# Kernel tuning notes

Measured on AMD Instinct MI355X. Metric: run time of the kernel, lower is better.

## Reference

```python
import jax, jax.numpy as jnp
import numpy as np

HID = 128
MAX_NODES = 100000
MAX_EDGES = 300000
EVT_LEN = 4096
NUM_NODE = 20000
NUM_EDGE = 320000
# EVENT_TYPE_ID_MAP: pad=0 start=1 end=2 node-add=3 node-delete=4 edge-add=5 edge-delete=6
NODE_ADD, NODE_DEL = 3, 4


def time_encode(t, time_w, time_b):
    # TimeEncoder: cos(Linear(1 -> hidden)(t))
    return jnp.cos(t[..., None] * time_w + time_b)


def gru_cell(x, h, w_ih, w_hh, b_ih, b_hh):
    gi = x @ w_ih.T + b_ih
    gh = h @ w_hh.T + b_hh
    i_r, i_z, i_n = jnp.split(gi, 3, axis=-1)
    h_r, h_z, h_n = jnp.split(gh, 3, axis=-1)
    r = jax.nn.sigmoid(i_r + h_r)
    z = jax.nn.sigmoid(i_z + h_z)
    n = jnp.tanh(i_n + r * h_n)
    return (1.0 - z) * n + z * h


def setup_inputs() -> dict:
    key = jax.random.key(0)
    ks = jax.random.split(key, 32)
    H = HID
    s = 0.05
    inp = {}
    inp["event_type_ids"] = jax.random.randint(ks[0], (EVT_LEN,), 0, 7)
    inp["src_ids"] = jax.random.randint(ks[1], (EVT_LEN,), 0, MAX_NODES)
    inp["src_mask"] = (jax.random.uniform(ks[2], (EVT_LEN,)) > 0.3).astype(jnp.float32)
    inp["dst_ids"] = jax.random.randint(ks[3], (EVT_LEN,), 0, MAX_NODES)
    inp["dst_mask"] = (jax.random.uniform(ks[4], (EVT_LEN,)) > 0.3).astype(jnp.float32)
    inp["event_edge_ids"] = jax.random.randint(ks[5], (EVT_LEN,), 0, MAX_EDGES)
    inp["event_embeddings"] = jax.random.normal(ks[6], (EVT_LEN, H), dtype=jnp.float32)
    inp["event_mask"] = (jax.random.uniform(ks[7], (EVT_LEN,)) > 0.2).astype(jnp.float32)
    inp["event_timestamps"] = jax.random.uniform(ks[8], (EVT_LEN,)) * 100.0
    inp["node_ids"] = jax.random.randint(ks[9], (NUM_NODE,), 0, MAX_NODES)
    inp["edge_ids"] = jax.random.randint(ks[10], (NUM_EDGE,), 0, MAX_EDGES)
    inp["edge_index"] = jax.random.randint(ks[11], (2, NUM_EDGE), 0, NUM_NODE)
    inp["time"] = 100
    # persistent-buffer state
    inp["memory"] = jax.random.normal(ks[12], (MAX_NODES, H), dtype=jnp.float32) * s
    inp["last_update"] = jax.random.uniform(ks[13], (MAX_EDGES,)) * 50.0
    inp["node_features"] = jax.random.normal(ks[14], (MAX_NODES, H), dtype=jnp.float32) * s
    inp["edge_features"] = jax.random.normal(ks[15], (MAX_EDGES, H), dtype=jnp.float32) * s
    # TimeEncoder params (Linear(1, H))
    inp["time_w"] = jax.random.normal(ks[16], (H,), dtype=jnp.float32) * s
    inp["time_b"] = jax.random.normal(ks[17], (H,), dtype=jnp.float32) * s
    # GRUCell(5H -> H)
    inp["gru_w_ih"] = jax.random.normal(ks[18], (3 * H, 5 * H), dtype=jnp.float32) * s
    inp["gru_w_hh"] = jax.random.normal(ks[19], (3 * H, H), dtype=jnp.float32) * s
    inp["gru_b_ih"] = jax.random.normal(ks[20], (3 * H,), dtype=jnp.float32) * s
    inp["gru_b_hh"] = jax.random.normal(ks[21], (3 * H,), dtype=jnp.float32) * s
    # TransformerConv(H, H, heads=1, edge_dim=2H)
    inp["wq"] = jax.random.normal(ks[22], (H, H), dtype=jnp.float32) * s
    inp["bq"] = jax.random.normal(ks[23], (H,), dtype=jnp.float32) * s
    inp["wk"] = jax.random.normal(ks[24], (H, H), dtype=jnp.float32) * s
    inp["bk"] = jax.random.normal(ks[25], (H,), dtype=jnp.float32) * s
    inp["wv"] = jax.random.normal(ks[26], (H, H), dtype=jnp.float32) * s
    inp["bv"] = jax.random.normal(ks[27], (H,), dtype=jnp.float32) * s
    inp["we"] = jax.random.normal(ks[28], (H, 2 * H), dtype=jnp.float32) * s  # lin_edge, no bias
    inp["wskip"] = jax.random.normal(ks[29], (H, H), dtype=jnp.float32) * s
    inp["bskip"] = jax.random.normal(ks[30], (H,), dtype=jnp.float32) * s
    return inp


def reference(event_type_ids, src_ids, src_mask, dst_ids, dst_mask, event_edge_ids,
              event_embeddings, event_mask, event_timestamps, node_ids, edge_ids,
              edge_index, time, memory, last_update, node_features, edge_features,
              time_w, time_b, gru_w_ih, gru_w_hh, gru_b_ih, gru_b_hh,
              wq, bq, wk, bk, wv, bv, we, wskip, bskip):
    H = HID
    # ---- message() ----
    L = event_type_ids.shape[0]
    type_embs = jnp.broadcast_to(event_type_ids[:, None].astype(memory.dtype), (L, H))
    src_embs = memory[src_ids] * src_mask[:, None]
    dst_embs = memory[dst_ids] * dst_mask[:, None]
    edge_last = last_update[event_edge_ids]
    rel_ts = event_timestamps - edge_last * dst_mask
    is_node_ev = ((event_type_ids == NODE_ADD) | (event_type_ids == NODE_DEL)).astype(event_timestamps.dtype)
    ts_emb = time_encode(event_timestamps * is_node_ev + rel_ts * dst_mask, time_w, time_b) * event_mask[:, None]
    src_msgs = jnp.concatenate([type_embs, src_embs, dst_embs, ts_emb, event_embeddings], axis=1) * event_mask[:, None]
    dst_msgs = jnp.concatenate([type_embs, dst_embs, src_embs, ts_emb, event_embeddings], axis=1) * dst_mask[:, None]
    # ---- agg_message(): scatter-mean over node ids ----
    def agg(msgs, ids):
        s = jax.ops.segment_sum(msgs, ids, num_segments=MAX_NODES)
        c = jax.ops.segment_sum(jnp.ones((msgs.shape[0],), msgs.dtype), ids, num_segments=MAX_NODES)
        return s / jnp.maximum(c, 1.0)[:, None]
    agg_src = agg(src_msgs, src_ids)
    agg_dst = agg(dst_msgs, dst_ids)
    # ---- GRU memory update on unique ids ----
    # torch: memory[cat(uniq_src, uniq_dst)] = rnn(...); reads use pre-update memory,
    # dst writes come after src writes so they override on overlap. Duplicate ids in
    # src_ids carry identical per-id values, so scatter-set is equivalent to unique().
    new_src = gru_cell(agg_src[src_ids], memory[src_ids], gru_w_ih, gru_w_hh, gru_b_ih, gru_b_hh)
    new_dst = gru_cell(agg_dst[dst_ids], memory[dst_ids], gru_w_ih, gru_w_hh, gru_b_ih, gru_b_hh)
    memory = memory.at[src_ids].set(new_src)
    memory = memory.at[dst_ids].set(new_dst)
    # ---- edge attributes ----
    rel_t = time - last_update[edge_ids]
    rel_t_embs = time_encode(rel_t, time_w, time_b)
    edge_attr = jnp.concatenate([rel_t_embs, edge_features[edge_ids]], axis=-1)  # (E, 2H)
    # ---- TransformerConv (heads=1, concat, root_weight) ----
    x = node_features[node_ids] + memory[node_ids]  # (N, H)
    src, dst = edge_index[0], edge_index[1]
    q = x @ wq.T + bq
    k = x @ wk.T + bk
    v = x @ wv.T + bv
    e = edge_attr @ we.T  # lin_edge (no bias)
    alpha = jnp.sum(q[dst] * (k[src] + e), axis=-1) / jnp.sqrt(jnp.asarray(H, x.dtype))
    amax = jax.ops.segment_max(alpha, dst, num_segments=x.shape[0])
    ex = jnp.exp(alpha - amax[dst])
    denom = jax.ops.segment_sum(ex, dst, num_segments=x.shape[0])
    p = ex / jnp.maximum(denom[dst], 1e-16)
    out = jax.ops.segment_sum(p[:, None] * (v[src] + e), dst, num_segments=x.shape[0])
    return out + x @ wskip.T + bskip
```

## Files before the change

### kernel.cpp

```cpp
#include <hip/hip_runtime.h>
#include <math.h>

#define HID   128
#define MAXN  100000
#define MAXE  300000
#define EVT   4096
#define NNODE 20000
#define NEDGE 320000

typedef unsigned short u16;
typedef __attribute__((ext_vector_type(8))) short bf16x8;
typedef __attribute__((ext_vector_type(4))) float f32x4;

#define OFF_WCATB     0u
#define OFF_WEB       589824u
#define OFF_WALLB     655360u
#define OFF_BALL      851968u
#define BASE2         855040u
#define OFF_HEAD_SRC  (BASE2 + 0u)
#define OFF_HEAD_DST  (BASE2 + 400128u)
#define OFF_CNT_SRC   (BASE2 + 800256u)
#define OFF_CNT_DST   (BASE2 + 1200384u)
#define OFF_CHAIN_SRC (BASE2 + 1600512u)
#define OFF_CHAIN_DST (BASE2 + 1616896u)
#define OFF_XHB       (BASE2 + 1703936u)
#define OFF_HG        (BASE2 + 14286848u)
#define OFF_GRZ       (BASE2 + 20000000u)
#define OFF_GIN       (BASE2 + 28388608u)
#define OFF_GHN       (BASE2 + 32582912u)
#define OFF_XB        (BASE2 + 20000000u)
#define OFF_QB        (BASE2 + 25120000u)
#define OFF_SKIPF     (BASE2 + 55840000u)
#define OFF_DEG       (BASE2 + 66080000u)
#define OFF_OFFS      (BASE2 + 66160128u)
#define OFF_CURSOR    (BASE2 + 66240256u)
#define OFF_SORTED    (BASE2 + 66320384u)
#define OFF_SACCB     (BASE2 + 67600384u)

__device__ __forceinline__ float sigmoidf_(float x) { return 1.f / (1.f + __expf(-x)); }
__device__ __forceinline__ u16 f2b(float f) {
    unsigned u = __float_as_uint(f);
    unsigned r = (u + 0x7fffu + ((u >> 16) & 1u)) >> 16;
    return (u16)r;
}
__device__ __forceinline__ float b2f(unsigned h) { return __uint_as_float(h << 16); }

__global__ void k_prep(const float* __restrict__ w_ih, const float* __restrict__ w_hh,
                       const float* __restrict__ we,
                       const float* __restrict__ wq, const float* __restrict__ wk_,
                       const float* __restrict__ wv, const float* __restrict__ wskip,
                       const float* __restrict__ bq, const float* __restrict__ bk,
                       const float* __restrict__ bv, const float* __restrict__ bskip,
                       u16* __restrict__ Wcatb, u16* __restrict__ we_b,
                       u16* __restrict__ Wallb, float* __restrict__ ball,
                       int* __restrict__ deg, char* __restrict__ zbase) {
    int b = blockIdx.x, t = threadIdx.x;
    if (b < 1152) {
        int idx = b * 256 + t;
        int row = idx / 768, col = idx % 768;
        float v = (col < 640) ? w_ih[row * 640 + col] : w_hh[row * 128 + (col - 640)];
        Wcatb[idx] = f2b(v);
        return;
    }
    b -= 1152;
    if (b < 128) {
        int i = b * 256 + t;
        we_b[i] = f2b(we[i]);
        return;
    }
    b -= 128;
    if (b < 79) {
        int i = b * 256 + t;
        if (i < NNODE) deg[i] = 0;
        return;
    }
    b -= 79;
    if (b < 384) {
        int idx = b * 256 + t;
        int row = idx >> 7;
        int k = idx & 127;
        float v;
        if (row < 128)      v = wq[row * 128 + k];
        else if (row < 256) v = wk_[(row - 128) * 128 + k];
        else if (row < 384) v = wv[(row - 256) * 128 + k];
        else if (row < 512) v = wskip[(row - 384) * 128 + k];
        else {
            int j = row - 512;
            float a = 0.f;
            for (int t2 = 0; t2 < 128; t2++) a += wq[t2 * 128 + k] * we[t2 * 256 + j];
            v = a;
        }
        Wallb[row * 128 + k] = f2b(v);
        if (k == 0) {
            float bb;
            if (row < 128)      bb = bq[row];
            else if (row < 256) bb = bk[row - 128];
            else if (row < 384) bb = bv[row - 256];
            else if (row < 512) bb = bskip[row - 384];
            else { int j = row - 512; float a = 0.f; for (int t2 = 0; t2 < 128; t2++) a += bq[t2] * we[t2 * 256 + j]; bb = a; }
            ball[row] = bb;
        }
        return;
    }
    b -= 384;
    const int NFF = 50016;
    uint4 ff = make_uint4(0xFFFFFFFFu, 0xFFFFFFFFu, 0xFFFFFFFFu, 0xFFFFFFFFu);
    uint4 zz = make_uint4(0u, 0u, 0u, 0u);
    int idx = b * 256 + t;
    int stride = 257 * 256;
    uint4* pff = (uint4*)zbase;
    uint4* pzz = (uint4*)(zbase + 800256);
    for (int i = idx; i < NFF; i += stride) pff[i] = ff;
    for (int i = idx; i < NFF; i += stride) pzz[i] = zz;
}

__global__ void k_msg_tables(const int* __restrict__ et_ids, const int* __restrict__ src_ids,
                          const float* __restrict__ src_mask, const int* __restrict__ dst_ids,
                          const float* __restrict__ dst_mask, const int* __restrict__ ev_eids,
                          const float* __restrict__ ev_emb, const float* __restrict__ ev_mask,
                          const float* __restrict__ ev_ts, const float* __restrict__ memory,
                          const float* __restrict__ last_update, const float* __restrict__ time_w,
                          const float* __restrict__ time_b,
                          int* __restrict__ head_src, int* __restrict__ head_dst,
                          int* __restrict__ cnt_src, int* __restrict__ cnt_dst,
                          int* __restrict__ chain_src, int* __restrict__ chain_dst,
                          const int* __restrict__ eidx, int* __restrict__ deg,
                          u16* __restrict__ XHb, float* __restrict__ Hg) {
    int b = blockIdx.x, t = threadIdx.x;
    if (b >= EVT) {
        int bb = b - EVT;
        if (bb < 32) {
            int i = bb * 128 + t;
            int s = src_ids[i], d = dst_ids[i];
            chain_src[i] = atomicExch(&head_src[s], i);
            atomicAdd(&cnt_src[s], 1);
            chain_dst[i] = atomicExch(&head_dst[d], i);
            atomicAdd(&cnt_dst[d], 1);
        } else {
            int j = (bb - 32) * 128 + t;
            atomicAdd(&deg[eidx[NEDGE + j]], 1);
        }
        return;
    }
    int i = b;
    int c = t;
    int et = et_ids[i];
    float sm = src_mask[i], dm = dst_mask[i], em = ev_mask[i], ts = ev_ts[i];
    int sid = src_ids[i], did = dst_ids[i], eid = ev_eids[i];
    float isnode = (et == 3 || et == 4) ? 1.f : 0.f;
    float rel = ts - last_update[eid] * dm;
    float tval = ts * isnode + rel * dm;
    float tse = __cosf(tval * time_w[c] + time_b[c]) * em;
    float typ = (float)et;
    float sv_raw = memory[(size_t)sid * HID + c];
    float dv_raw = memory[(size_t)did * HID + c];
    float sv = sv_raw * sm;
    float dv = dv_raw * dm;
    float ev = ev_emb[(size_t)i * HID + c];
    Hg[(size_t)i * HID + c] = sv_raw;
    Hg[(size_t)(EVT + i) * HID + c] = dv_raw;
    u16* xs = XHb + (size_t)i * 768;
    xs[c] = f2b(typ * em); xs[128 + c] = f2b(sv * em); xs[256 + c] = f2b(dv * em);
    xs[384 + c] = f2b(tse * em); xs[512 + c] = f2b(ev * em);
    xs[640 + c] = f2b(sv_raw);
    u16* xd = XHb + (size_t)(EVT + i) * 768;
    xd[c] = f2b(typ * dm); xd[128 + c] = f2b(dv * dm); xd[256 + c] = f2b(sv * dm);
    xd[384 + c] = f2b(tse * dm); xd[512 + c] = f2b(ev * dm);
    xd[640 + c] = f2b(dv_raw);
}

__global__ void k_fix(const int* __restrict__ src_ids, const int* __restrict__ dst_ids,
                      const int* __restrict__ head_src, const int* __restrict__ head_dst,
                      const int* __restrict__ chain_src, const int* __restrict__ chain_dst,
                      const int* __restrict__ cnt_src, const int* __restrict__ cnt_dst,
                      const int* __restrict__ et_ids, const float* __restrict__ src_mask,
                      const float* __restrict__ dst_mask, const int* __restrict__ ev_eids,
                      const float* __restrict__ ev_emb, const float* __restrict__ ev_mask,
                      const float* __restrict__ ev_ts, const float* __restrict__ memory,
                      const float* __restrict__ last_update, const float* __restrict__ time_w,
                      const float* __restrict__ time_b, u16* __restrict__ XHb) {
    int r = blockIdx.x, c = threadIdx.x;
    bool is_src = (r < EVT);
    int id = is_src ? src_ids[r] : dst_ids[r - EVT];
    int cnt = is_src ? cnt_src[id] : cnt_dst[id];
    if (cnt < 2) return;
    float own = memory[(size_t)id * HID + c];
    float tw = time_w[c], tb = time_b[c];
    float a0 = 0.f, a1 = 0.f, a2 = 0.f, a3 = 0.f, a4 = 0.f;
    int j = is_src ? head_src[id] : head_dst[id];
    for (int k = 0; k < cnt; ++k) {
        int et = et_ids[j];
        float sm = src_mask[j], dm = dst_mask[j], em = ev_mask[j], ts = ev_ts[j];
        int eid = ev_eids[j];
        float isnode = (et == 3 || et == 4) ? 1.f : 0.f;
        float rel = ts - last_update[eid] * dm;
        float tval = ts * isnode + rel * dm;
        float tse = __cosf(tval * tw + tb);
        float ev = ev_emb[(size_t)j * HID + c];
        float typ = (float)et;
        if (is_src) {
            float sv = own * sm;
            float dv = memory[(size_t)dst_ids[j] * HID + c] * dm;
            float tsm = tse * em;
            a0 += typ * em; a1 += sv * em; a2 += dv * em;
            a3 += tsm * em; a4 += ev * em;
            j = chain_src[j];
        } else {
            float dv = own * dm;
            float sv = memory[(size_t)src_ids[j] * HID + c] * sm;
            float tsm = tse * em;
            a0 += typ * dm; a1 += dv * dm; a2 += sv * dm;
            a3 += tsm * dm; a4 += ev * dm;
            j = chain_dst[j];
        }
    }
    float inv = 1.f / (float)cnt;
    u16* x = XHb + (size_t)r * 768;
    x[c] = f2b(a0 * inv); x[128 + c] = f2b(a1 * inv); x[256 + c] = f2b(a2 * inv);
    x[384 + c] = f2b(a3 * inv); x[512 + c] = f2b(a4 * inv);
}

__device__ __forceinline__ void gate_pass(const u16* __restrict__ A, int lda,
                                          const u16* __restrict__ W, int ldw, int K,
                                          f32x4 acc[4][4], u16* Als, u16* Wls,
                                          int bm, int wm, int wn, int l15, int quad, int tid) {
    for (int k0 = 0; k0 < K; k0 += 32) {
#pragma unroll
        for (int h = 0; h < 2; ++h) {
            int ch = tid + h * 256;
            int row = ch >> 2, kc = (ch & 3) * 8;
            *(float4*)&Als[row * 40 + kc] = *(const float4*)(A + (size_t)(bm + row) * lda + k0 + kc);
            *(float4*)&Wls[row * 40 + kc] = *(const float4*)(W + (size_t)row * ldw + k0 + kc);
        }
        __syncthreads();
        bf16x8 af[4], bfr[4];
#pragma unroll
        for (int r = 0; r < 4; ++r)
            af[r] = *(const bf16x8*)&Als[(wm + r * 16 + l15) * 40 + quad * 8];
#pragma unroll
        for (int c2 = 0; c2 < 4; ++c2)
            bfr[c2] = *(const bf16x8*)&Wls[(wn + c2 * 16 + l15) * 40 + quad * 8];
#pragma unroll
        for (int r = 0; r < 4; ++r)
#pragma unroll
            for (int c2 = 0; c2 < 4; ++c2)
                acc[r][c2] = __builtin_amdgcn_mfma_f32_16x16x32_bf16(af[r], bfr[c2], acc[r][c2], 0, 0, 0);
        __syncthreads();
    }
}

__global__ __launch_bounds__(256) void k_gemm_gates(const u16* __restrict__ XHb,
        const u16* __restrict__ Wcat, const float* __restrict__ b_ih,
        const float* __restrict__ b_hh, float* __restrict__ Grz,
        float* __restrict__ Gin, float* __restrict__ Ghn) {
    __shared__ u16 Als[128 * 40];
    __shared__ u16 Wls[128 * 40];
    int tid = threadIdx.x;
    int bm = blockIdx.x * 128;
    int g = blockIdx.y;
    int wave = tid >> 6, lane = tid & 63;
    int wm = (wave & 1) * 64, wn = (wave >> 1) * 64;
    int l15 = lane & 15, quad = lane >> 4;
    f32x4 acc_i[4][4] = {};
    f32x4 acc_h[4][4] = {};
    const u16* Wg = Wcat + (size_t)(g * 128) * 768;
    gate_pass(XHb, 768, Wg, 768, 640, acc_i, Als, Wls, bm, wm, wn, l15, quad, tid);
    gate_pass(XHb + 640, 768, Wg + 640, 768, 128, acc_h, Als, Wls, bm, wm, wn, l15, quad, tid);
#pragma unroll
    for (int r = 0; r < 4; ++r) {
#pragma unroll
        for (int c2 = 0; c2 < 4; ++c2) {
            int ncol = wn + c2 * 16 + l15;
            float bi = b_ih[g * 128 + ncol];
            float bh = b_hh[g * 128 + ncol];
#pragma unroll
            for (int reg = 0; reg < 4; ++reg) {
                int mrow = bm + wm + r * 16 + quad * 4 + reg;
                if (g < 2) {
                    Grz[(size_t)mrow * 256 + g * 128 + ncol] =
                        acc_i[r][c2][reg] + acc_h[r][c2][reg] + bi + bh;
                } else {
                    Gin[(size_t)mrow * 128 + ncol] = acc_i[r][c2][reg] + bi;
                    Ghn[(size_t)mrow * 128 + ncol] = acc_h[r][c2][reg] + bh;
                }
            }
        }
    }
}

__global__ void k_gru_scatter(const float* __restrict__ Grz, const float* __restrict__ Gin,
                              const float* __restrict__ Ghn, const float* __restrict__ Hg,
                              const int* __restrict__ src_ids, const int* __restrict__ dst_ids,
                              const int* __restrict__ cnt_dst, float* __restrict__ memory) {
    int r = blockIdx.x, c = threadIdx.x;
    float rg = sigmoidf_(Grz[(size_t)r * 256 + c]);
    float z  = sigmoidf_(Grz[(size_t)r * 256 + 128 + c]);
    float n  = tanhf(Gin[(size_t)r * 128 + c] + rg * Ghn[(size_t)r * 128 + c]);
    float h0 = Hg[(size_t)r * HID + c];
    float h  = (1.f - z) * n + z * h0;
    if (r < EVT) {
        int sid = src_ids[r];
        if (cnt_dst[sid] == 0) memory[(size_t)sid * HID + c] = h;
    } else {
        int did = dst_ids[r - EVT];
        memory[(size_t)did * HID + c] = h;
    }
}

__device__ __forceinline__ void gemm_tile(const u16* __restrict__ A, const u16* __restrict__ W,
                                          const float* __restrict__ bias, float* __restrict__ C,
                                          int M, int N, int K, int acc,
                                          u16* Als, u16* Wls) {
    int tid = threadIdx.x;
    int bm = blockIdx.x * 128, bn = blockIdx.y * 128;
    int wave = tid >> 6, lane = tid & 63;
    int wm = (wave & 1) * 64, wn = (wave >> 1) * 64;
    int l15 = lane & 15, quad = lane >> 4;
    f32x4 accf[4][4] = {};
    for (int k0 = 0; k0 < K; k0 += 32) {
#pragma unroll
        for (int h = 0; h < 2; ++h) {
            int ch = tid + h * 256;
            int row = ch >> 2, kc = (ch & 3) * 8;
            int gr = bm + row;
            float4 av = make_float4(0.f, 0.f, 0.f, 0.f);
            if (gr < M) av = *(const float4*)(A + (size_t)gr * K + k0 + kc);
            *(float4*)&Als[row * 40 + kc] = av;
            int wr = bn + row;
            float4 wv_ = *(const float4*)(W + (size_t)wr * K + k0 + kc);
            *(float4*)&Wls[row * 40 + kc] = wv_;
        }
        __syncthreads();
        bf16x8 af[4], bfr[4];
#pragma unroll
        for (int r = 0; r < 4; ++r)
            af[r] = *(const bf16x8*)&Als[(wm + r * 16 + l15) * 40 + quad * 8];
#pragma unroll
        for (int c2 = 0; c2 < 4; ++c2)
            bfr[c2] = *(const bf16x8*)&Wls[(wn + c2 * 16 + l15) * 40 + quad * 8];
#pragma unroll
        for (int r = 0; r < 4; ++r)
#pragma unroll
            for (int c2 = 0; c2 < 4; ++c2)
                accf[r][c2] = __builtin_amdgcn_mfma_f32_16x16x32_bf16(af[r], bfr[c2], accf[r][c2], 0, 0, 0);
        __syncthreads();
    }
#pragma unroll
    for (int r = 0; r < 4; ++r) {
#pragma unroll
        for (int c2 = 0; c2 < 4; ++c2) {
            int ncol = bn + wn + c2 * 16 + l15;
            float bv = bias ? bias[ncol] : 0.f;
#pragma unroll
            for (int reg = 0; reg < 4; ++reg) {
                int mrow = bm + wm + r * 16 + quad * 4 + reg;
                if (mrow >= M) continue;
                float v = accf[r][c2][reg] + bv;
                if (acc) v += C[(size_t)mrow * N + ncol];
                C[(size_t)mrow * N + ncol] = v;
            }
        }
    }
}

__global__ __launch_bounds__(256) void k_gemm_mfma(const u16* __restrict__ A,
                                                   const u16* __restrict__ W,
                                                   const float* __restrict__ bias,
                                                   float* __restrict__ C,
                                                   int M, int N, int K, int acc) {
    __shared__ u16 Als[128 * 40];
    __shared__ u16 Wls[128 * 40];
    gemm_tile(A, W, bias, C, M, N, K, acc, Als, Wls);
}

__global__ __launch_bounds__(256) void k_gemm_qkvse(const u16* __restrict__ A,
                                                    const u16* __restrict__ W,
                                                    const float* __restrict__ bias,
                                                    u16* __restrict__ QB,
                                                    float* __restrict__ SkipF,
                                                    const int* __restrict__ eidx,
                                                    int* __restrict__ cursor,
                                                    int* __restrict__ sorted) {
    __shared__ u16 Als[128 * 40];
    __shared__ u16 Wls[128 * 40];
    if (blockIdx.y == 6) {
        int j = blockIdx.x * 256 + threadIdx.x;
        for (; j < NEDGE; j += 157 * 256) {
            int d = eidx[NEDGE + j];
            int pos = atomicAdd(&cursor[d], 1);
            sorted[pos] = j;
        }
        return;
    }
    int tid = threadIdx.x;
    int bm = blockIdx.x * 128, bn = blockIdx.y * 128;
    int wave = tid >> 6, lane = tid & 63;
    int wm = (wave & 1) * 64, wn = (wave >> 1) * 64;
    int l15 = lane & 15, quad = lane >> 4;
    f32x4 accf[4][4] = {};
    for (int k0 = 0; k0 < 128; k0 += 32) {
#pragma unroll
        for (int h = 0; h < 2; ++h) {
            int ch = tid + h * 256;
            int row = ch >> 2, kc = (ch & 3) * 8;
            int gr = bm + row;
            float4 av = make_float4(0.f, 0.f, 0.f, 0.f);
            if (gr < NNODE) av = *(const float4*)(A + (size_t)gr * 128 + k0 + kc);
            *(float4*)&Als[row * 40 + kc] = av;
            int wr = bn + row;
            float4 wv_ = *(const float4*)(W + (size_t)wr * 128 + k0 + kc);
            *(float4*)&Wls[row * 40 + kc] = wv_;
        }
        __syncthreads();
        bf16x8 af[4], bfr[4];
#pragma unroll
        for (int r = 0; r < 4; ++r)
            af[r] = *(const bf16x8*)&Als[(wm + r * 16 + l15) * 40 + quad * 8];
#pragma unroll
        for (int c2 = 0; c2 < 4; ++c2)
            bfr[c2] = *(const bf16x8*)&Wls[(wn + c2 * 16 + l15) * 40 + quad * 8];
#pragma unroll
        for (int r = 0; r < 4; ++r)
#pragma unroll
            for (int c2 = 0; c2 < 4; ++c2)
                accf[r][c2] = __builtin_amdgcn_mfma_f32_16x16x32_bf16(af[r], bfr[c2], accf[r][c2], 0, 0, 0);
        __syncthreads();
    }
#pragma unroll
    for (int r = 0; r < 4; ++r) {
#pragma unroll
        for (int c2 = 0; c2 < 4; ++c2) {
            int ncol = bn + wn + c2 * 16 + l15;
            float bv = bias[ncol];
#pragma unroll
            for (int reg = 0; reg < 4; ++reg) {
                int mrow = bm + wm + r * 16 + quad * 4 + reg;
                if (mrow >= NNODE) continue;
                float v = accf[r][c2][reg] + bv;
                QB[(size_t)mrow * 768 + ncol] = f2b(v);
                if (ncol >= 384 && ncol < 512)
                    SkipF[(size_t)mrow * 128 + (ncol - 384)] = v;
            }
        }
    }
}

__global__ __launch_bounds__(1024) void k_x_scan(const int* __restrict__ node_ids,
                                                 const float* __restrict__ nf,
                                                 const float* __restrict__ memory,
                                                 u16* __restrict__ Xb,
                                                 const int* __restrict__ deg,
                                                 int* __restrict__ offs,
                                                 int* __restrict__ cursor) {
    __shared__ int wsum[16];
    int p = blockIdx.x, t = threadIdx.x;
    if (p < 2500) {
        int row = p * 8 + (t >> 7), c = t & 127;
        int nid = node_ids[row];
        Xb[(size_t)row * HID + c] = f2b(nf[(size_t)nid * HID + c] + memory[(size_t)nid * HID + c]);
        return;
    }
    int lane = t & 63, w = t >> 6;
    int carry = 0;
    const int N4 = NNODE / 4;
    for (int base = 0; base < N4; base += 1024) {
        int i4 = base + t;
        int4 v = make_int4(0, 0, 0, 0);
        if (i4 < N4) v = ((const int4*)deg)[i4];
        int s = v.x + v.y + v.z + v.w;
        int x = s;
#pragma unroll
        for (int d = 1; d < 64; d <<= 1) { int y = __shfl_up(x, d, 64); if (lane >= d) x += y; }
        if (lane == 63) wsum[w] = x;
        __syncthreads();
        int add = 0, tot = 0;
        for (int k2 = 0; k2 < 16; ++k2) { int ss = wsum[k2]; if (k2 < w) add += ss; tot += ss; }
        if (i4 < N4) {
            int e = carry + add + x - s;
            int4 o;
            o.x = e;
            o.y = e + v.x;
            o.z = o.y + v.y;
            o.w = o.z + v.z;
            ((int4*)offs)[i4] = o;
            ((int4*)cursor)[i4] = o;
        }
        carry += tot;
        __syncthreads();
    }
    if (t == 0) offs[NNODE] = NEDGE;
}

__global__ __launch_bounds__(256) void k_node(const u16* __restrict__ QB,
        const float* __restrict__ SkipF, const int* __restrict__ offs,
        const int* __restrict__ sorted, const int* __restrict__ eidx,
        const int* __restrict__ edge_ids, const float* __restrict__ last_update,
        const float* __restrict__ time_w, const float* __restrict__ time_b,
        const float* __restrict__ ef, const int* __restrict__ tptr,
        float* __restrict__ out, u16* __restrict__ saccb) {
    int wave = threadIdx.x >> 6, lane = threadIdx.x & 63;
    int n = blockIdx.x * 4 + wave;
    int c = 2 * lane;
    const u16* rowq = QB + (size_t)n * 768;
    unsigned qw  = *(const unsigned*)(rowq + c);
    unsigned qtw = *(const unsigned*)(rowq + 512 + c);
    unsigned qfw = *(const unsigned*)(rowq + 640 + c);
    float2 qd, qet, qef;
    qd.x  = b2f(qw & 0xffffu);  qd.y  = b2f(qw >> 16);
    qet.x = b2f(qtw & 0xffffu); qet.y = b2f(qtw >> 16);
    qef.x = b2f(qfw & 0xffffu); qef.y = b2f(qfw >> 16);
    float2 skip = *(const float2*)(SkipF + (size_t)n * HID + c);
    float2 tw   = *(const float2*)(time_w + c);
    float2 tb   = *(const float2*)(time_b + c);
    float tf = (float)(*tptr);
    int start = offs[n], end = offs[n + 1];
    int deg = end - start;
    if (deg == 0) {
        *(float2*)(out + (size_t)n * HID + c) = skip;
        *(unsigned*)(saccb + (size_t)n * 256 + c) = 0u;
        *(unsigned*)(saccb + (size_t)n * 256 + 128 + c) = 0u;
        return;
    }
    float m = -1e30f, l_ = 0.f;
    float va0 = 0.f, va1 = 0.f, s00 = 0.f, s01 = 0.f, s10 = 0.f, s11 = 0.f;
    for (int cb = start; cb < end; cb += 64) {
        int cnt = end - cb; if (cnt > 64) cnt = 64;
        int s_l = 0, eid_l = 0; float rt_l = 0.f;
        if (lane < cnt) {
            int j = sorted[cb + lane];
            s_l = eidx[j];
            eid_l = edge_ids[j];
            rt_l = tf - last_update[eid_l];
        }
        for (int e0 = 0; e0 < cnt; e0 += 4) {
            float pv[4], cv0[4], cv1[4], vx[4], vy[4], ex[4], ey[4];
#pragma unroll
            for (int i = 0; i < 4; ++i) {
                int idx = e0 + i;
                int sel = (idx < cnt) ? idx : e0;
                int s   = __shfl(s_l, sel, 64);
                int eid = __shfl(eid_l, sel, 64);
                float rt = __shfl(rt_l, sel, 64);
                unsigned kvp = *(const unsigned*)(QB + (size_t)s * 768 + 128 + c);
                unsigned vvp = *(const unsigned*)(QB + (size_t)s * 768 + 256 + c);
                float2 ev = *(const float2*)(ef + (size_t)eid * HID + c);
                float k0f = b2f(kvp & 0xffffu), k1f = b2f(kvp >> 16);
                vx[i] = b2f(vvp & 0xffffu); vy[i] = b2f(vvp >> 16);
                cv0[i] = __cosf(rt * tw.x + tb.x);
                cv1[i] = __cosf(rt * tw.y + tb.y);
                ex[i] = ev.x; ey[i] = ev.y;
                pv[i] = qd.x * k0f + qd.y * k1f + qet.x * cv0[i] + qet.y * cv1[i]
                      + qef.x * ev.x + qef.y * ev.y;
            }
#pragma unroll
            for (int msk = 32; msk > 0; msk >>= 1) {
#pragma unroll
                for (int i = 0; i < 4; ++i) pv[i] += __shfl_xor(pv[i], msk, 64);
            }
            float al[4];
#pragma unroll
            for (int i = 0; i < 4; ++i)
                al[i] = (e0 + i < cnt) ? pv[i] * 0.08838834764831845f : -1e30f;
            float gm = fmaxf(fmaxf(al[0], al[1]), fmaxf(al[2], al[3]));
            if (gm > m) {
                float fac = __expf(m - gm);
                l_ *= fac; va0 *= fac; va1 *= fac;
                s00 *= fac; s01 *= fac; s10 *= fac; s11 *= fac;
                m = gm;
            }
#pragma unroll
            for (int i = 0; i < 4; ++i) {
                float w = __expf(al[i] - m);
                l_ += w;
                va0 += w * vx[i]; va1 += w * vy[i];
                s00 += w * cv0[i]; s01 += w * cv1[i];
                s10 += w * ex[i]; s11 += w * ey[i];
            }
        }
    }
    float inv = 1.f / fmaxf(l_, 1e-16f);
    float2 o; o.x = va0 * inv + skip.x; o.y = va1 * inv + skip.y;
    *(float2*)(out + (size_t)n * HID + c) = o;
    unsigned p0 = (unsigned)f2b(s00 * inv) | ((unsigned)f2b(s01 * inv) << 16);
    unsigned p1 = (unsigned)f2b(s10 * inv) | ((unsigned)f2b(s11 * inv) << 16);
    *(unsigned*)(saccb + (size_t)n * 256 + c) = p0;
    *(unsigned*)(saccb + (size_t)n * 256 + 128 + c) = p1;
}

extern "C" void kernel_launch(void* const* d_in, const int* in_sizes, int n_in,
                              void* d_out, int out_size, void* d_ws, size_t ws_size,
                              hipStream_t stream) {
    const int*   et_ids        = (const int*)d_in[0];
    const int*   src_ids       = (const int*)d_in[1];
    const float* src_mask      = (const float*)d_in[2];
    const int*   dst_ids       = (const int*)d_in[3];
    const float* dst_mask      = (const float*)d_in[4];
    const int*   ev_eids       = (const int*)d_in[5];
    const float* ev_emb        = (const float*)d_in[6];
    const float* ev_mask       = (const float*)d_in[7];
    const float* ev_ts         = (const float*)d_in[8];
    const int*   node_ids      = (const int*)d_in[9];
    const int*   edge_ids      = (const int*)d_in[10];
    const int*   edge_index    = (const int*)d_in[11];
    const int*   tptr          = (const int*)d_in[12];
    float*       memory        = (float*)d_in[13];
    const float* last_update   = (const float*)d_in[14];
    const float* node_features = (const float*)d_in[15];
    const float* edge_features = (const float*)d_in[16];
    const float* time_w        = (const float*)d_in[17];
    const float* time_b        = (const float*)d_in[18];
    const float* w_ih          = (const float*)d_in[19];
    const float* w_hh          = (const float*)d_in[20];
    const float* b_ih          = (const float*)d_in[21];
    const float* b_hh          = (const float*)d_in[22];
    const float* wq            = (const float*)d_in[23];
    const float* bq            = (const float*)d_in[24];
    const float* wk            = (const float*)d_in[25];
    const float* bk            = (const float*)d_in[26];
    const float* wv            = (const float*)d_in[27];
    const float* bv            = (const float*)d_in[28];
    const float* we            = (const float*)d_in[29];
    const float* wskip         = (const float*)d_in[30];
    const float* bskip         = (const float*)d_in[31];
    float* out = (float*)d_out;
    char*  wsb = (char*)d_ws;

    u16*   Wcatb    = (u16*)(wsb + OFF_WCATB);
    u16*   we_b     = (u16*)(wsb + OFF_WEB);
    u16*   Wallb    = (u16*)(wsb + OFF_WALLB);
    float* ball     = (float*)(wsb + OFF_BALL);
    int*   head_src = (int*)(wsb + OFF_HEAD_SRC);
    int*   head_dst = (int*)(wsb + OFF_HEAD_DST);
    int*   cnt_src  = (int*)(wsb + OFF_CNT_SRC);
    int*   cnt_dst  = (int*)(wsb + OFF_CNT_DST);
    int*   chain_src= (int*)(wsb + OFF_CHAIN_SRC);
    int*   chain_dst= (int*)(wsb + OFF_CHAIN_DST);
    u16*   XHb      = (u16*)(wsb + OFF_XHB);
    float* Hg       = (float*)(wsb + OFF_HG);
    float* Grz      = (float*)(wsb + OFF_GRZ);
    float* Gin      = (float*)(wsb + OFF_GIN);
    float* Ghn      = (float*)(wsb + OFF_GHN);
    u16*   Xb       = (u16*)(wsb + OFF_XB);
    u16*   QB       = (u16*)(wsb + OFF_QB);
    float* SkipF    = (float*)(wsb + OFF_SKIPF);
    int*   deg      = (int*)(wsb + OFF_DEG);
    int*   offs     = (int*)(wsb + OFF_OFFS);
    int*   cursor   = (int*)(wsb + OFF_CURSOR);
    int*   sorted   = (int*)(wsb + OFF_SORTED);
    u16*   saccb    = (u16*)(wsb + OFF_SACCB);

    k_prep<<<2000, 256, 0, stream>>>(w_ih, w_hh, we, wq, wk, wv, wskip, bq, bk, bv, bskip,
                                     Wcatb, we_b, Wallb, ball, deg, wsb + OFF_HEAD_SRC);
    k_msg_tables<<<6628, 128, 0, stream>>>(et_ids, src_ids, src_mask, dst_ids, dst_mask, ev_eids,
                                           ev_emb, ev_mask, ev_ts, memory, last_update, time_w, time_b,
                                           head_src, head_dst, cnt_src, cnt_dst, chain_src, chain_dst,
                                           edge_index, deg, XHb, Hg);
    k_fix<<<2 * EVT, 128, 0, stream>>>(src_ids, dst_ids, head_src, head_dst, chain_src, chain_dst,
                                       cnt_src, cnt_dst, et_ids, src_mask, dst_mask, ev_eids,
                                       ev_emb, ev_mask, ev_ts, memory, last_update, time_w, time_b,
                                       XHb);
    k_gemm_gates<<<dim3(64, 3), 256, 0, stream>>>(XHb, Wcatb, b_ih, b_hh, Grz, Gin, Ghn);
    k_gru_scatter<<<2 * EVT, 128, 0, stream>>>(Grz, Gin, Ghn, Hg, src_ids, dst_ids, cnt_dst, memory);
    k_x_scan<<<2501, 1024, 0, stream>>>(node_ids, node_features, memory, Xb, deg, offs, cursor);
    k_gemm_qkvse<<<dim3(157, 7), 256, 0, stream>>>(Xb, Wallb, ball, QB, SkipF,
                                                   edge_index, cursor, sorted);
    k_node<<<NNODE / 4, 256, 0, stream>>>(QB, SkipF, offs, sorted, edge_index, edge_ids,
                                          last_update, time_w, time_b, edge_features, tptr,
                                          out, saccb);
    k_gemm_mfma<<<dim3(157, 1), 256, 0, stream>>>(saccb, we_b, nullptr, out, NNODE, 128, 256, 1);
}
```

Before: 480.8 us.

## Move skip projection from QKV GEMM into final edge-projection GEMM

```diff
diff --git a/kernel.cpp b/kernel.cpp
--- a/kernel.cpp
+++ b/kernel.cpp
@@ -15,7 +15,8 @@
 #define OFF_WCATB     0u
 #define OFF_WEB       589824u
 #define OFF_WALLB     655360u
-#define OFF_BALL      851968u
+#define OFF_BALL      819200u
+#define OFF_WSKIPB    821760u
 #define BASE2         855040u
 #define OFF_HEAD_SRC  (BASE2 + 0u)
 #define OFF_HEAD_DST  (BASE2 + 400128u)
@@ -30,7 +31,6 @@
 #define OFF_GHN       (BASE2 + 32582912u)
 #define OFF_XB        (BASE2 + 20000000u)
 #define OFF_QB        (BASE2 + 25120000u)
-#define OFF_SKIPF     (BASE2 + 55840000u)
 #define OFF_DEG       (BASE2 + 66080000u)
 #define OFF_OFFS      (BASE2 + 66160128u)
 #define OFF_CURSOR    (BASE2 + 66240256u)
@@ -50,9 +50,10 @@
                        const float* __restrict__ wq, const float* __restrict__ wk_,
                        const float* __restrict__ wv, const float* __restrict__ wskip,
                        const float* __restrict__ bq, const float* __restrict__ bk,
-                       const float* __restrict__ bv, const float* __restrict__ bskip,
+                       const float* __restrict__ bv,
                        u16* __restrict__ Wcatb, u16* __restrict__ we_b,
                        u16* __restrict__ Wallb, float* __restrict__ ball,
+                       u16* __restrict__ wskipb,
                        int* __restrict__ deg, char* __restrict__ zbase) {
     int b = blockIdx.x, t = threadIdx.x;
     if (b < 1152) {
@@ -75,7 +76,7 @@
         return;
     }
     b -= 79;
-    if (b < 384) {
+    if (b < 320) {
         int idx = b * 256 + t;
         int row = idx >> 7;
         int k = idx & 127;
@@ -83,9 +84,8 @@
         if (row < 128)      v = wq[row * 128 + k];
         else if (row < 256) v = wk_[(row - 128) * 128 + k];
         else if (row < 384) v = wv[(row - 256) * 128 + k];
-        else if (row < 512) v = wskip[(row - 384) * 128 + k];
         else {
-            int j = row - 512;
+            int j = row - 384;
             float a = 0.f;
             for (int t2 = 0; t2 < 128; t2++) a += wq[t2 * 128 + k] * we[t2 * 256 + j];
             v = a;
@@ -96,13 +96,18 @@
             if (row < 128)      bb = bq[row];
             else if (row < 256) bb = bk[row - 128];
             else if (row < 384) bb = bv[row - 256];
-            else if (row < 512) bb = bskip[row - 384];
-            else { int j = row - 512; float a = 0.f; for (int t2 = 0; t2 < 128; t2++) a += bq[t2] * we[t2 * 256 + j]; bb = a; }
+            else { int j = row - 384; float a = 0.f; for (int t2 = 0; t2 < 128; t2++) a += bq[t2] * we[t2 * 256 + j]; bb = a; }
             ball[row] = bb;
         }
         return;
     }
-    b -= 384;
+    b -= 320;
+    if (b < 64) {
+        int i = b * 256 + t;
+        wskipb[i] = f2b(wskip[i]);
+        return;
+    }
+    b -= 64;
     const int NFF = 50016;
     uint4 ff = make_uint4(0xFFFFFFFFu, 0xFFFFFFFFu, 0xFFFFFFFFu, 0xFFFFFFFFu);
     uint4 zz = make_uint4(0u, 0u, 0u, 0u);
@@ -307,83 +312,16 @@
     }
 }
 
-__device__ __forceinline__ void gemm_tile(const u16* __restrict__ A, const u16* __restrict__ W,
-                                          const float* __restrict__ bias, float* __restrict__ C,
-                                          int M, int N, int K, int acc,
-                                          u16* Als, u16* Wls) {
-    int tid = threadIdx.x;
-    int bm = blockIdx.x * 128, bn = blockIdx.y * 128;
-    int wave = tid >> 6, lane = tid & 63;
-    int wm = (wave & 1) * 64, wn = (wave >> 1) * 64;
-    int l15 = lane & 15, quad = lane >> 4;
-    f32x4 accf[4][4] = {};
-    for (int k0 = 0; k0 < K; k0 += 32) {
-#pragma unroll
-        for (int h = 0; h < 2; ++h) {
-            int ch = tid + h * 256;
-            int row = ch >> 2, kc = (ch & 3) * 8;
-            int gr = bm + row;
-            float4 av = make_float4(0.f, 0.f, 0.f, 0.f);
-            if (gr < M) av = *(const float4*)(A + (size_t)gr * K + k0 + kc);
-            *(float4*)&Als[row * 40 + kc] = av;
-            int wr = bn + row;
-            float4 wv_ = *(const float4*)(W + (size_t)wr * K + k0 + kc);
-            *(float4*)&Wls[row * 40 + kc] = wv_;
-        }
-        __syncthreads();
-        bf16x8 af[4], bfr[4];
-#pragma unroll
-        for (int r = 0; r < 4; ++r)
-            af[r] = *(const bf16x8*)&Als[(wm + r * 16 + l15) * 40 + quad * 8];
-#pragma unroll
-        for (int c2 = 0; c2 < 4; ++c2)
-            bfr[c2] = *(const bf16x8*)&Wls[(wn + c2 * 16 + l15) * 40 + quad * 8];
-#pragma unroll
-        for (int r = 0; r < 4; ++r)
-#pragma unroll
-            for (int c2 = 0; c2 < 4; ++c2)
-                accf[r][c2] = __builtin_amdgcn_mfma_f32_16x16x32_bf16(af[r], bfr[c2], accf[r][c2], 0, 0, 0);
-        __syncthreads();
-    }
-#pragma unroll
-    for (int r = 0; r < 4; ++r) {
-#pragma unroll
-        for (int c2 = 0; c2 < 4; ++c2) {
-            int ncol = bn + wn + c2 * 16 + l15;
-            float bv = bias ? bias[ncol] : 0.f;
-#pragma unroll
-            for (int reg = 0; reg < 4; ++reg) {
-                int mrow = bm + wm + r * 16 + quad * 4 + reg;
-                if (mrow >= M) continue;
-                float v = accf[r][c2][reg] + bv;
-                if (acc) v += C[(size_t)mrow * N + ncol];
-                C[(size_t)mrow * N + ncol] = v;
-            }
-        }
-    }
-}
-
-__global__ __launch_bounds__(256) void k_gemm_mfma(const u16* __restrict__ A,
-                                                   const u16* __restrict__ W,
-                                                   const float* __restrict__ bias,
-                                                   float* __restrict__ C,
-                                                   int M, int N, int K, int acc) {
-    __shared__ u16 Als[128 * 40];
-    __shared__ u16 Wls[128 * 40];
-    gemm_tile(A, W, bias, C, M, N, K, acc, Als, Wls);
-}
-
 __global__ __launch_bounds__(256) void k_gemm_qkvse(const u16* __restrict__ A,
                                                     const u16* __restrict__ W,
                                                     const float* __restrict__ bias,
                                                     u16* __restrict__ QB,
-                                                    float* __restrict__ SkipF,
                                                     const int* __restrict__ eidx,
                                                     int* __restrict__ cursor,
                                                     int* __restrict__ sorted) {
     __shared__ u16 Als[128 * 40];
     __shared__ u16 Wls[128 * 40];
-    if (blockIdx.y == 6) {
+    if (blockIdx.y == 5) {
         int j = blockIdx.x * 256 + threadIdx.x;
         for (; j < NEDGE; j += 157 * 256) {
             int d = eidx[NEDGE + j];
@@ -436,10 +374,7 @@
             for (int reg = 0; reg < 4; ++reg) {
                 int mrow = bm + wm + r * 16 + quad * 4 + reg;
                 if (mrow >= NNODE) continue;
-                float v = accf[r][c2][reg] + bv;
-                QB[(size_t)mrow * 768 + ncol] = f2b(v);
-                if (ncol >= 384 && ncol < 512)
-                    SkipF[(size_t)mrow * 128 + (ncol - 384)] = v;
+                QB[(size_t)mrow * 640 + ncol] = f2b(accf[r][c2][reg] + bv);
             }
         }
     }
@@ -492,7 +427,7 @@
 }
 
 __global__ __launch_bounds__(256) void k_node(const u16* __restrict__ QB,
-        const float* __restrict__ SkipF, const int* __restrict__ offs,
+        const int* __restrict__ offs,
         const int* __restrict__ sorted, const int* __restrict__ eidx,
         const int* __restrict__ edge_ids, const float* __restrict__ last_update,
         const float* __restrict__ time_w, const float* __restrict__ time_b,
@@ -501,22 +436,22 @@
     int wave = threadIdx.x >> 6, lane = threadIdx.x & 63;
     int n = blockIdx.x * 4 + wave;
     int c = 2 * lane;
-    const u16* rowq = QB + (size_t)n * 768;
+    const u16* rowq = QB + (size_t)n * 640;
     unsigned qw  = *(const unsigned*)(rowq + c);
-    unsigned qtw = *(const unsigned*)(rowq + 512 + c);
-    unsigned qfw = *(const unsigned*)(rowq + 640 + c);
+    unsigned qtw = *(const unsigned*)(rowq + 384 + c);
+    unsigned qfw = *(const unsigned*)(rowq + 512 + c);
     float2 qd, qet, qef;
     qd.x  = b2f(qw & 0xffffu);  qd.y  = b2f(qw >> 16);
     qet.x = b2f(qtw & 0xffffu); qet.y = b2f(qtw >> 16);
     qef.x = b2f(qfw & 0xffffu); qef.y = b2f(qfw >> 16);
-    float2 skip = *(const float2*)(SkipF + (size_t)n * HID + c);
     float2 tw   = *(const float2*)(time_w + c);
     float2 tb   = *(const float2*)(time_b + c);
     float tf = (float)(*tptr);
     int start = offs[n], end = offs[n + 1];
     int deg = end - start;
     if (deg == 0) {
-        *(float2*)(out + (size_t)n * HID + c) = skip;
+        float2 zz; zz.x = 0.f; zz.y = 0.f;
+        *(float2*)(out + (size_t)n * HID + c) = zz;
         *(unsigned*)(saccb + (size_t)n * 256 + c) = 0u;
         *(unsigned*)(saccb + (size_t)n * 256 + 128 + c) = 0u;
         return;
@@ -541,8 +476,8 @@
                 int s   = __shfl(s_l, sel, 64);
                 int eid = __shfl(eid_l, sel, 64);
                 float rt = __shfl(rt_l, sel, 64);
-                unsigned kvp = *(const unsigned*)(QB + (size_t)s * 768 + 128 + c);
-                unsigned vvp = *(const unsigned*)(QB + (size_t)s * 768 + 256 + c);
+                unsigned kvp = *(const unsigned*)(QB + (size_t)s * 640 + 128 + c);
+                unsigned vvp = *(const unsigned*)(QB + (size_t)s * 640 + 256 + c);
                 float2 ev = *(const float2*)(ef + (size_t)eid * HID + c);
                 float k0f = b2f(kvp & 0xffffu), k1f = b2f(kvp >> 16);
                 vx[i] = b2f(vvp & 0xffffu); vy[i] = b2f(vvp >> 16);
@@ -579,12 +514,75 @@
         }
     }
     float inv = 1.f / fmaxf(l_, 1e-16f);
-    float2 o; o.x = va0 * inv + skip.x; o.y = va1 * inv + skip.y;
+    float2 o; o.x = va0 * inv; o.y = va1 * inv;
     *(float2*)(out + (size_t)n * HID + c) = o;
     unsigned p0 = (unsigned)f2b(s00 * inv) | ((unsigned)f2b(s01 * inv) << 16);
     unsigned p1 = (unsigned)f2b(s10 * inv) | ((unsigned)f2b(s11 * inv) << 16);
     *(unsigned*)(saccb + (size_t)n * 256 + c) = p0;
     *(unsigned*)(saccb + (size_t)n * 256 + 128 + c) = p1;
+}
+
+__global__ __launch_bounds__(256) void k_final(const u16* __restrict__ saccb,
+                                               const u16* __restrict__ Xb,
+                                               const u16* __restrict__ web,
+                                               const u16* __restrict__ wskipb,
+                                               const float* __restrict__ bskip,
+                                               float* __restrict__ out) {
+    __shared__ u16 Als[128 * 40];
+    __shared__ u16 Wls[128 * 40];
+    int tid = threadIdx.x;
+    int bm = blockIdx.x * 128;
+    int wave = tid >> 6, lane = tid & 63;
+    int wm = (wave & 1) * 64, wn = (wave >> 1) * 64;
+    int l15 = lane & 15, quad = lane >> 4;
+    f32x4 accf[4][4] = {};
+#pragma unroll
+    for (int pass = 0; pass < 2; ++pass) {
+        const u16* A = pass ? Xb : saccb;
+        const u16* W = pass ? wskipb : web;
+        int lda = pass ? 128 : 256;
+        int K = pass ? 128 : 256;
+        for (int k0 = 0; k0 < K; k0 += 32) {
+#pragma unroll
+            for (int h = 0; h < 2; ++h) {
+                int ch = tid + h * 256;
+                int row = ch >> 2, kc = (ch & 3) * 8;
+                int gr = bm + row;
+                float4 av = make_float4(0.f, 0.f, 0.f, 0.f);
+                if (gr < NNODE) av = *(const float4*)(A + (size_t)gr * lda + k0 + kc);
+                *(float4*)&Als[row * 40 + kc] = av;
+                *(float4*)&Wls[row * 40 + kc] = *(const float4*)(W + (size_t)row * lda + k0 + kc);
+            }
+            __syncthreads();
+            bf16x8 af[4], bfr[4];
+#pragma unroll
+            for (int r = 0; r < 4; ++r)
+                af[r] = *(const bf16x8*)&Als[(wm + r * 16 + l15) * 40 + quad * 8];
+#pragma unroll
+            for (int c2 = 0; c2 < 4; ++c2)
+                bfr[c2] = *(const bf16x8*)&Wls[(wn + c2 * 16 + l15) * 40 + quad * 8];
+#pragma unroll
+            for (int r = 0; r < 4; ++r)
+#pragma unroll
+                for (int c2 = 0; c2 < 4; ++c2)
+                    accf[r][c2] = __builtin_amdgcn_mfma_f32_16x16x32_bf16(af[r], bfr[c2], accf[r][c2], 0, 0, 0);
+            __syncthreads();
+        }
+    }
+#pragma unroll
+    for (int r = 0; r < 4; ++r) {
+#pragma unroll
+        for (int c2 = 0; c2 < 4; ++c2) {
+            int ncol = wn + c2 * 16 + l15;
+            float bv = bskip[ncol];
+#pragma unroll
+            for (int reg = 0; reg < 4; ++reg) {
+                int mrow = bm + wm + r * 16 + quad * 4 + reg;
+                if (mrow >= NNODE) continue;
+                out[(size_t)mrow * HID + ncol] += accf[r][c2][reg] + bv;
+            }
+        }
+    }
 }
 
 extern "C" void kernel_launch(void* const* d_in, const int* in_sizes, int n_in,
@@ -629,6 +627,7 @@
     u16*   we_b     = (u16*)(wsb + OFF_WEB);
     u16*   Wallb    = (u16*)(wsb + OFF_WALLB);
     float* ball     = (float*)(wsb + OFF_BALL);
+    u16*   wskipb   = (u16*)(wsb + OFF_WSKIPB);
     int*   head_src = (int*)(wsb + OFF_HEAD_SRC);
     int*   head_dst = (int*)(wsb + OFF_HEAD_DST);
     int*   cnt_src  = (int*)(wsb + OFF_CNT_SRC);
@@ -642,15 +641,14 @@
     float* Ghn      = (float*)(wsb + OFF_GHN);
     u16*   Xb       = (u16*)(wsb + OFF_XB);
     u16*   QB       = (u16*)(wsb + OFF_QB);
-    float* SkipF    = (float*)(wsb + OFF_SKIPF);
     int*   deg      = (int*)(wsb + OFF_DEG);
     int*   offs     = (int*)(wsb + OFF_OFFS);
     int*   cursor   = (int*)(wsb + OFF_CURSOR);
     int*   sorted   = (int*)(wsb + OFF_SORTED);
     u16*   saccb    = (u16*)(wsb + OFF_SACCB);
 
-    k_prep<<<2000, 256, 0, stream>>>(w_ih, w_hh, we, wq, wk, wv, wskip, bq, bk, bv, bskip,
-                                     Wcatb, we_b, Wallb, ball, deg, wsb + OFF_HEAD_SRC);
+    k_prep<<<2000, 256, 0, stream>>>(w_ih, w_hh, we, wq, wk, wv, wskip, bq, bk, bv,
+                                     Wcatb, we_b, Wallb, ball, wskipb, deg, wsb + OFF_HEAD_SRC);
     k_msg_tables<<<6628, 128, 0, stream>>>(et_ids, src_ids, src_mask, dst_ids, dst_mask, ev_eids,
                                            ev_emb, ev_mask, ev_ts, memory, last_update, time_w, time_b,
                                            head_src, head_dst, cnt_src, cnt_dst, chain_src, chain_dst,
@@ -662,10 +660,10 @@
     k_gemm_gates<<<dim3(64, 3), 256, 0, stream>>>(XHb, Wcatb, b_ih, b_hh, Grz, Gin, Ghn);
     k_gru_scatter<<<2 * EVT, 128, 0, stream>>>(Grz, Gin, Ghn, Hg, src_ids, dst_ids, cnt_dst, memory);
     k_x_scan<<<2501, 1024, 0, stream>>>(node_ids, node_features, memory, Xb, deg, offs, cursor);
-    k_gemm_qkvse<<<dim3(157, 7), 256, 0, stream>>>(Xb, Wallb, ball, QB, SkipF,
+    k_gemm_qkvse<<<dim3(157, 6), 256, 0, stream>>>(Xb, Wallb, ball, QB,
                                                    edge_index, cursor, sorted);
-    k_node<<<NNODE / 4, 256, 0, stream>>>(QB, SkipF, offs, sorted, edge_index, edge_ids,
+    k_node<<<NNODE / 4, 256, 0, stream>>>(QB, offs, sorted, edge_index, edge_ids,
                                           last_update, time_w, time_b, edge_features, tptr,
                                           out, saccb);
-    k_gemm_mfma<<<dim3(157, 1), 256, 0, stream>>>(saccb, we_b, nullptr, out, NNODE, 128, 256, 1);
-}
+    k_final<<<157, 256, 0, stream>>>(saccb, Xb, we_b, wskipb, bskip, out);
+}
```

Result: no change. 473.7 us (-1.5%).
